# Kernel optimization log

Measured on AMD Instinct MI355X. Metric: run time of the kernel, lower is better.

The kernel has to match this reference:

```python
import jax, jax.numpy as jnp
import numpy as np

N_USERS = 100000
N_ITEMS = 50000
N_NODES = N_USERS + N_ITEMS
D = 64
N_INTENTS = 128
N_LAYERS = 2
E = 3200000
E_U = 1600000
E_I = 800000
N_MP = 2


def spmm(idx, vals, x, n):
    # sparse (n,n) COO @ dense (n,d): out[r] = sum_e vals[e] * x[c[e]] where idx=[rows;cols]
    return jax.ops.segment_sum(vals[:, None] * x[idx[1]], idx[0], num_segments=n)


def graph_conv_both(edges, h, n):
    # DGL GraphConv(norm='both', weight=None, bias=None, allow_zero_in_degree=True)
    src, dst = edges[0], edges[1]
    ones = jnp.ones(src.shape[0], h.dtype)
    deg_out = jax.ops.segment_sum(ones, src, num_segments=n)
    deg_in = jax.ops.segment_sum(ones, dst, num_segments=n)
    inv = lambda d: jnp.where(d > 0, jax.lax.rsqrt(jnp.maximum(d, 1e-12)), 0.0)
    hs = h * inv(deg_out)[:, None]
    agg = jax.ops.segment_sum(hs[src], dst, num_segments=n)
    return agg * inv(deg_in)[:, None]


def semantic_attention(z, W1, b1, w2):
    # z: (N, M, D)
    w = jnp.tanh(z @ W1 + b1) @ w2        # (N, M)
    beta = jax.nn.softmax(w.mean(0))       # (M,)
    return jnp.einsum('m,nmd->nd', beta, z)


def dccf(G_indices, G_values, feat_user, feat_item, user_intent, item_intent):
    emb = jnp.concatenate([feat_user, feat_item], axis=0)
    total = emb
    cur = emb
    for _ in range(N_LAYERS):
        gnn = spmm(G_indices, G_values, cur, N_NODES)
        u, it = cur[:N_USERS], cur[N_USERS:]
        u_int = jax.nn.softmax(u @ user_intent, axis=1) @ user_intent.T
        i_int = jax.nn.softmax(it @ item_intent, axis=1) @ item_intent.T
        cur = gnn + jnp.concatenate([u_int, i_int], axis=0) + cur
        total = total + cur
    return total[:N_USERS], total[N_USERS:]


def han(mp_edges, h, n, W1, b1, w2):
    z = jnp.stack([graph_conv_both(mp_edges[m], h, n) for m in range(N_MP)], axis=1)
    return semantic_attention(z, W1, b1, w2)


def setup_inputs() -> dict:
    key = jax.random.key(0)
    ks = jax.random.split(key, 16)
    s = 1.0 / np.sqrt(D)
    return {
        'G_indices': jax.random.randint(ks[0], (2, E), 0, N_NODES),
        'G_values': jax.random.uniform(ks[1], (E,), jnp.float32),
        'feat_user': jax.random.normal(ks[2], (N_USERS, D), jnp.float32) * s,
        'feat_item': jax.random.normal(ks[3], (N_ITEMS, D), jnp.float32) * s,
        'user_intent': jax.random.normal(ks[4], (D, N_INTENTS), jnp.float32) * s,
        'item_intent': jax.random.normal(ks[5], (D, N_INTENTS), jnp.float32) * s,
        'mp_user_edges': jax.random.randint(ks[6], (N_MP, 2, E_U), 0, N_USERS),
        'mp_item_edges': jax.random.randint(ks[7], (N_MP, 2, E_I), 0, N_ITEMS),
        'sem_user_W1': jax.random.normal(ks[8], (D, 128), jnp.float32) * s,
        'sem_user_b1': jnp.zeros((128,), jnp.float32),
        'sem_user_w2': jax.random.normal(ks[9], (128,), jnp.float32) * s,
        'sem_item_W1': jax.random.normal(ks[10], (D, 128), jnp.float32) * s,
        'sem_item_b1': jnp.zeros((128,), jnp.float32),
        'sem_item_w2': jax.random.normal(ks[11], (128,), jnp.float32) * s,
        'user_idx': jax.random.randint(ks[12], (1024,), 0, N_USERS),
        'item_idx': jax.random.randint(ks[13], (1024,), 0, N_ITEMS),
        'neg_item_idx': jax.random.randint(ks[14], (1024,), 0, N_ITEMS),
    }


def reference(G_indices, G_values, feat_user, feat_item, user_intent, item_intent,
              mp_user_edges, mp_item_edges,
              sem_user_W1, sem_user_b1, sem_user_w2,
              sem_item_W1, sem_item_b1, sem_item_w2,
              user_idx, item_idx, neg_item_idx):
    ua, ia = dccf(G_indices, G_values, feat_user, feat_item, user_intent, item_intent)
    h_user = han(mp_user_edges, feat_user, N_USERS, sem_user_W1, sem_user_b1, sem_user_w2)
    h_item = han(mp_item_edges, feat_item, N_ITEMS, sem_item_W1, sem_item_b1, sem_item_w2)
    user_emb = 0.5 * ua + 0.5 * h_user
    item_emb = 0.5 * ia + 0.5 * h_item
    return (user_emb, item_emb)
```

## Files before the change

### kernel.cpp

```cpp
#include <hip/hip_runtime.h>
#include <hip/hip_bf16.h>
#include <hip/hip_fp16.h>
#include <math.h>

#define N_USERS 100000
#define N_ITEMS 50000
#define N_NODES 150000
#define DD 64
#define E_G 3200000
#define EU 1600000
#define EI 800000
#define E_HAN 4800000
#define NH 300000
#define NBG 293
#define NBH 586
#define ROWS 32

__device__ __forceinline__ float invdeg(float d){
  return d > 0.f ? rsqrtf(fmaxf(d, 1e-12f)) : 0.f;
}
__device__ __forceinline__ float tanh_fast(float x){
  float cx = fminf(15.f, fmaxf(-15.f, x));
  float t = __expf(2.f*cx);
  return (t - 1.f)/(t + 1.f);
}
__device__ __forceinline__ unsigned short f2b(float x){
  unsigned int b = __float_as_uint(x);
  b += 0x7FFFu + ((b >> 16) & 1u);
  return (unsigned short)(b >> 16);
}
__device__ __forceinline__ float b2f(unsigned short u){
  return __uint_as_float(((unsigned int)u) << 16);
}
__device__ __forceinline__ float b2f_lo(unsigned int u){
  return __uint_as_float(u << 16);
}
__device__ __forceinline__ float b2f_hi(unsigned int u){
  return __uint_as_float(u & 0xFFFF0000u);
}
__device__ __forceinline__ unsigned short f2h(float x){
  return __half_as_ushort(__float2half(x));
}
__device__ __forceinline__ float h2f(unsigned short u){
  return __half2float(__ushort_as_half(u));
}
__device__ __forceinline__ float2 h2x2(unsigned int u){
  __half2 h = *reinterpret_cast<__half2*>(&u);
  return __half22float2(h);
}

__global__ void k_init(const float* __restrict__ fu, const float* __restrict__ fi,
                       float* __restrict__ cur, unsigned short* __restrict__ curh,
                       float* __restrict__ total){
  int i = blockIdx.x*256 + threadIdx.x;
  if (i >= N_NODES*DD) return;
  float v = (i < N_USERS*DD) ? fu[i] : fi[i - N_USERS*DD];
  cur[i] = v; total[i] = v; curh[i] = f2h(v);
}

__global__ __launch_bounds__(256) void k_colscan(int* __restrict__ wh, int nb,
                                                 int* __restrict__ colsum){
  __shared__ int s[256];
  int b = blockIdx.x, tid = threadIdx.x;
  int v = wh[tid*nb + b];
  s[tid] = v; __syncthreads();
  for (int o = 1; o < 256; o <<= 1){
    int t = (tid >= o) ? s[tid - o] : 0;
    __syncthreads();
    s[tid] += t;
    __syncthreads();
  }
  wh[tid*nb + b] = s[tid] - v;
  if (tid == 255) colsum[b] = s[255];
}

__global__ __launch_bounds__(256) void k_bscan(const int* __restrict__ colsum, int nb,
                                               int total, int* __restrict__ bB){
  __shared__ int s[256];
  __shared__ int carry;
  int tid = threadIdx.x;
  if (tid == 0) carry = 0;
  __syncthreads();
  for (int base = 0; base < nb; base += 256){
    int i = base + tid;
    int v = (i < nb) ? colsum[i] : 0;
    s[tid] = v; __syncthreads();
    for (int o = 1; o < 256; o <<= 1){
      int t = (tid >= o) ? s[tid - o] : 0;
      __syncthreads();
      s[tid] += t;
      __syncthreads();
    }
    int c = carry;
    if (i < nb) bB[i] = c + s[tid] - v;
    __syncthreads();
    if (tid == 255) carry = c + s[255];
    __syncthreads();
  }
  if (tid == 0) bB[nb] = total;
}

__global__ __launch_bounds__(256) void k_h1_g(const int* __restrict__ gi,
                                              int* __restrict__ wh){
  __shared__ int h[NBG];
  int tid = threadIdx.x;
  for (int b = tid; b < NBG; b += 256) h[b] = 0;
  __syncthreads();
  int e0 = blockIdx.x*(E_G/256);
  for (int i = tid; i < E_G/256; i += 256)
    atomicAdd(&h[gi[e0 + i] >> 9], 1);
  __syncthreads();
  for (int b = tid; b < NBG; b += 256) wh[blockIdx.x*NBG + b] = h[b];
}

__global__ __launch_bounds__(256) void k_h2_g(const int* __restrict__ gi,
        const float* __restrict__ gv, const int* __restrict__ wh,
        const int* __restrict__ bB, uint2* __restrict__ kv){
  __shared__ int lcur[NBG];
  int tid = threadIdx.x, wg = blockIdx.x;
  for (int b = tid; b < NBG; b += 256) lcur[b] = bB[b] + wh[wg*NBG + b];
  __syncthreads();
  int e0 = wg*(E_G/256);
  for (int i = tid; i < E_G/256; i += 256){
    int e = e0 + i;
    int d = gi[e];
    int p = atomicAdd(&lcur[d >> 9], 1);
    uint2 r;
    r.x = ((unsigned)(d & 511) << 18) | (unsigned)gi[E_G + e];
    r.y = __float_as_uint(gv[e]);
    kv[p] = r;
  }
}

__global__ __launch_bounds__(256) void k_p2_g(const int* __restrict__ bB,
        const uint2* __restrict__ kv, int* __restrict__ off,
        unsigned int* __restrict__ packed){
  __shared__ int cnt[512], sc[512], lcur[512];
  int b = blockIdx.x, tid = threadIdx.x;
  int d0 = b << 9;
  int dcnt = min(512, N_NODES - d0);
  int pb = bB[b], pe = bB[b+1];
  for (int i = tid; i < 512; i += 256) cnt[i] = 0;
  __syncthreads();
  for (int p = pb + tid; p < pe; p += 256)
    atomicAdd(&cnt[kv[p].x >> 18], 1);
  __syncthreads();
  sc[tid] = cnt[tid]; sc[tid + 256] = cnt[tid + 256];
  __syncthreads();
  for (int o = 1; o < 512; o <<= 1){
    int a0 = (tid >= o) ? sc[tid - o] : 0;
    int a1 = sc[tid + 256 - o];
    __syncthreads();
    sc[tid] += a0; sc[tid + 256] += a1;
    __syncthreads();
  }
  for (int i = tid; i < 512; i += 256) lcur[i] = pb + sc[i] - cnt[i];
  for (int i = tid; i < dcnt; i += 256) off[d0 + i] = pb + sc[i] - cnt[i];
  if (tid == 0) off[d0 + dcnt] = pe;
  __syncthreads();
  for (int p = pb + tid; p < pe; p += 256){
    uint2 r = kv[p];
    int dl = (int)(r.x >> 18);
    unsigned int s = r.x & 0x3FFFFu;
    float v = __uint_as_float(r.y);
    int q14 = (int)(v*16383.f + 0.5f);
    if (q14 > 16383) q14 = 16383;
    int q = atomicAdd(&lcur[dl], 1);
    packed[q] = (s << 14) | (unsigned int)q14;
  }
}

__global__ __launch_bounds__(256) void k_spmm_gp(const int* __restrict__ off,
        const unsigned int* __restrict__ packed,
        const unsigned short* __restrict__ curh, unsigned short* __restrict__ gnnh){
  int wv = threadIdx.x >> 6, lane = threadIdx.x & 63;
  int node = blockIdx.x*4 + wv;
  if (node >= N_NODES) return;
  int b = off[node], e = off[node+1];
  int c8 = (lane & 7)*8, sl = lane >> 3;
  const float inv14 = 1.f/16383.f;
  float a[8];
  #pragma unroll
  for (int j = 0; j < 8; ++j) a[j] = 0.f;
  for (int k = b; k < e; k += 16){
    int i0 = k + sl, i1 = i0 + 8;
    unsigned int pk0 = (i0 < e) ? packed[i0] : 0u;
    unsigned int pk1 = (i1 < e) ? packed[i1] : 0u;
    int s0 = (int)(pk0 >> 14), s1 = (int)(pk1 >> 14);
    float w0 = (float)(pk0 & 16383u) * inv14;
    float w1 = (float)(pk1 & 16383u) * inv14;
    const uint4 u0 = *(const uint4*)&curh[s0*DD + c8];
    const uint4 u1 = *(const uint4*)&curh[s1*DD + c8];
    float2 f;
    f = h2x2(u0.x); a[0]=fmaf(w0,f.x,a[0]); a[1]=fmaf(w0,f.y,a[1]);
    f = h2x2(u0.y); a[2]=fmaf(w0,f.x,a[2]); a[3]=fmaf(w0,f.y,a[3]);
    f = h2x2(u0.z); a[4]=fmaf(w0,f.x,a[4]); a[5]=fmaf(w0,f.y,a[5]);
    f = h2x2(u0.w); a[6]=fmaf(w0,f.x,a[6]); a[7]=fmaf(w0,f.y,a[7]);
    f = h2x2(u1.x); a[0]=fmaf(w1,f.x,a[0]); a[1]=fmaf(w1,f.y,a[1]);
    f = h2x2(u1.y); a[2]=fmaf(w1,f.x,a[2]); a[3]=fmaf(w1,f.y,a[3]);
    f = h2x2(u1.z); a[4]=fmaf(w1,f.x,a[4]); a[5]=fmaf(w1,f.y,a[5]);
    f = h2x2(u1.w); a[6]=fmaf(w1,f.x,a[6]); a[7]=fmaf(w1,f.y,a[7]);
  }
  #pragma unroll
  for (int j = 0; j < 8; ++j){
    a[j] += __shfl_xor(a[j], 8, 64);
    a[j] += __shfl_xor(a[j], 16, 64);
    a[j] += __shfl_xor(a[j], 32, 64);
  }
  if (lane < 8){
    uint4 o;
    o.x = (unsigned)f2h(a[0]) | ((unsigned)f2h(a[1]) << 16);
    o.y = (unsigned)f2h(a[2]) | ((unsigned)f2h(a[3]) << 16);
    o.z = (unsigned)f2h(a[4]) | ((unsigned)f2h(a[5]) << 16);
    o.w = (unsigned)f2h(a[6]) | ((unsigned)f2h(a[7]) << 16);
    *(uint4*)&gnnh[node*DD + c8] = o;
  }
}

__global__ __launch_bounds__(256) void k_intent2(const float* __restrict__ intent,
        const unsigned short* __restrict__ gnnh, float* __restrict__ cur,
        unsigned short* __restrict__ curh, float* __restrict__ total,
        int base, int nrows){
  __shared__ float sB[64*132];
  __shared__ float sU[ROWS*132];
  int tid = threadIdx.x, tx = tid & 15, ty = tid >> 4;

  for (int i = tid; i < 2048; i += 256){
    int r = i >> 5, c = (i & 31) << 2;
    *(float4*)&sB[r*132 + c] = *(const float4*)&intent[r*128 + c];
  }
  {
    int r = tid & 31, q0 = tid >> 5;
    int rr = blockIdx.x*ROWS + r;
    int rowg = base + (rr < nrows ? rr : nrows - 1);
    for (int q = q0; q < 16; q += 8){
      float4 v = *(const float4*)&cur[rowg*DD + 4*q];
      sU[(4*q+0)*36 + r] = v.x;
      sU[(4*q+1)*36 + r] = v.y;
      sU[(4*q+2)*36 + r] = v.z;
      sU[(4*q+3)*36 + r] = v.w;
    }
  }
  __syncthreads();

  float w[2][8];
  #pragma unroll
  for (int i = 0; i < 2; ++i)
    #pragma unroll
    for (int k = 0; k < 8; ++k) w[i][k] = 0.f;
  for (int d = 0; d < 64; ++d){
    float2 a = *(const float2*)&sU[d*36 + 2*ty];
    float4 b0 = *(const float4*)&sB[d*132 + 8*tx];
    float4 b1 = *(const float4*)&sB[d*132 + 8*tx + 4];
    float bb[8] = {b0.x,b0.y,b0.z,b0.w,b1.x,b1.y,b1.z,b1.w};
    #pragma unroll
    for (int k = 0; k < 8; ++k){ w[0][k] += a.x*bb[k]; w[1][k] += a.y*bb[k]; }
  }

  float p[2][8];
  #pragma unroll
  for (int i = 0; i < 2; ++i){
    float mx = w[i][0];
    #pragma unroll
    for (int k = 1; k < 8; ++k) mx = fmaxf(mx, w[i][k]);
    mx = fmaxf(mx, __shfl_xor(mx, 1, 64));
    mx = fmaxf(mx, __shfl_xor(mx, 2, 64));
    mx = fmaxf(mx, __shfl_xor(mx, 4, 64));
    mx = fmaxf(mx, __shfl_xor(mx, 8, 64));
    float s = 0.f;
    #pragma unroll
    for (int k = 0; k < 8; ++k){ p[i][k] = __expf(w[i][k] - mx); s += p[i][k]; }
    s += __shfl_xor(s, 1, 64);
    s += __shfl_xor(s, 2, 64);
    s += __shfl_xor(s, 4, 64);
    s += __shfl_xor(s, 8, 64);
    float inv = 1.f / s;
    #pragma unroll
    for (int k = 0; k < 8; ++k) p[i][k] *= inv;
  }
  __syncthreads();
  #pragma unroll
  for (int i = 0; i < 2; ++i){
    *(float4*)&sU[(2*ty+i)*132 + 8*tx]     = make_float4(p[i][0],p[i][1],p[i][2],p[i][3]);
    *(float4*)&sU[(2*ty+i)*132 + 8*tx + 4] = make_float4(p[i][4],p[i][5],p[i][6],p[i][7]);
  }
  __syncthreads();

  float o[2][4];
  #pragma unroll
  for (int i = 0; i < 2; ++i)
    #pragma unroll
    for (int m = 0; m < 4; ++m) o[i][m] = 0.f;
  for (int q = 0; q < 32; ++q){
    float4 p0 = *(const float4*)&sU[(2*ty+0)*132 + 4*q];
    float4 p1 = *(const float4*)&sU[(2*ty+1)*132 + 4*q];
    #pragma unroll
    for (int m = 0; m < 4; ++m){
      float4 bl = *(const float4*)&sB[(4*tx+m)*132 + 4*q];
      o[0][m] += p0.x*bl.x + p0.y*bl.y + p0.z*bl.z + p0.w*bl.w;
      o[1][m] += p1.x*bl.x + p1.y*bl.y + p1.z*bl.z + p1.w*bl.w;
    }
  }

  #pragma unroll
  for (int i = 0; i < 2; ++i){
    int rr = blockIdx.x*ROWS + 2*ty + i;
    if (rr < nrows){
      int rowg = base + rr;
      ushort4 gh = *(const ushort4*)&gnnh[rowg*DD + 4*tx];
      float4 c = *(const float4*)&cur[rowg*DD + 4*tx];
      float4 t = *(const float4*)&total[rowg*DD + 4*tx];
      float4 cn = make_float4(h2f(gh.x) + o[i][0] + c.x, h2f(gh.y) + o[i][1] + c.y,
                              h2f(gh.z) + o[i][2] + c.z, h2f(gh.w) + o[i][3] + c.w);
      *(float4*)&cur[rowg*DD + 4*tx] = cn;
      ushort4 ch;
      ch.x = f2h(cn.x); ch.y = f2h(cn.y); ch.z = f2h(cn.z); ch.w = f2h(cn.w);
      *(ushort4*)&curh[rowg*DD + 4*tx] = ch;
      *(float4*)&total[rowg*DD + 4*tx] =
          make_float4(t.x + cn.x, t.y + cn.y, t.z + cn.z, t.w + cn.w);
    }
  }
}

__device__ __forceinline__ void han_decode(int t, const int* mp_u, const int* mp_i,
                                           int* gs, int* gd){
  if (t < 2*EU){
    int s = (t < EU) ? 0 : 1;
    int e = t - s*EU;
    const int* sp = mp_u + (long)s*2*EU;
    int nb = s*N_USERS;
    *gs = nb + sp[e]; *gd = nb + sp[EU + e];
  } else {
    int t2 = t - 2*EU;
    int s = (t2 < EI) ? 0 : 1;
    int e = t2 - s*EI;
    const int* sp = mp_i + (long)s*2*EI;
    int nb = 2*N_USERS + s*N_ITEMS;
    *gs = nb + sp[e]; *gd = nb + sp[EI + e];
  }
}

__global__ __launch_bounds__(256) void k_h1_h(const int* __restrict__ mp_u,
        const int* __restrict__ mp_i, int* __restrict__ whD, int* __restrict__ whS){
  __shared__ int hd[NBH], hs[NBH];
  int tid = threadIdx.x;
  for (int b = tid; b < NBH; b += 256){ hd[b] = 0; hs[b] = 0; }
  __syncthreads();
  int t0 = blockIdx.x*(E_HAN/256);
  for (int i = tid; i < E_HAN/256; i += 256){
    int gs, gd;
    han_decode(t0 + i, mp_u, mp_i, &gs, &gd);
    atomicAdd(&hd[gd >> 9], 1);
    atomicAdd(&hs[gs >> 9], 1);
  }
  __syncthreads();
  for (int b = tid; b < NBH; b += 256){
    whD[blockIdx.x*NBH + b] = hd[b];
    whS[blockIdx.x*NBH + b] = hs[b];
  }
}

__global__ __launch_bounds__(256) void k_h2_h(const int* __restrict__ mp_u,
        const int* __restrict__ mp_i, const int* __restrict__ whD,
        const int* __restrict__ whS, const int* __restrict__ bBD,
        const int* __restrict__ bBS, unsigned int* __restrict__ keyD,
        int* __restrict__ keyS){
  __shared__ int lcD[NBH], lcS[NBH];
  int tid = threadIdx.x, wg = blockIdx.x;
  for (int b = tid; b < NBH; b += 256){
    lcD[b] = bBD[b] + whD[wg*NBH + b];
    lcS[b] = bBS[b] + whS[wg*NBH + b];
  }
  __syncthreads();
  int t0 = wg*(E_HAN/256);
  for (int i = tid; i < E_HAN/256; i += 256){
    int gs, gd;
    han_decode(t0 + i, mp_u, mp_i, &gs, &gd);
    int pD = atomicAdd(&lcD[gd >> 9], 1);
    keyD[pD] = ((unsigned)(gd & 511) << 19) | (unsigned)gs;
    int pS = atomicAdd(&lcS[gs >> 9], 1);
    keyS[pS] = gs;
  }
}

__global__ __launch_bounds__(256) void k_p2_h(const int* __restrict__ bB,
        const unsigned int* __restrict__ key, const int* __restrict__ dego,
        int* __restrict__ off, unsigned int* __restrict__ ssrc){
  __shared__ int cnt[512], sc[512], lcur[512];
  int b = blockIdx.x, tid = threadIdx.x;
  int d0 = b << 9;
  int dcnt = min(512, NH - d0);
  int pb = bB[b], pe = bB[b+1];
  for (int i = tid; i < 512; i += 256) cnt[i] = 0;
  __syncthreads();
  for (int p = pb + tid; p < pe; p += 256)
    atomicAdd(&cnt[key[p] >> 19], 1);
  __syncthreads();
  sc[tid] = cnt[tid]; sc[tid + 256] = cnt[tid + 256];
  __syncthreads();
  for (int o = 1; o < 512; o <<= 1){
    int a0 = (tid >= o) ? sc[tid - o] : 0;
    int a1 = sc[tid + 256 - o];
    __syncthreads();
    sc[tid] += a0; sc[tid + 256] += a1;
    __syncthreads();
  }
  for (int i = tid; i < 512; i += 256) lcur[i] = pb + sc[i] - cnt[i];
  for (int i = tid; i < dcnt; i += 256) off[d0 + i] = pb + sc[i] - cnt[i];
  if (tid == 0) off[d0 + dcnt] = pe;
  __syncthreads();
  for (int p = pb + tid; p < pe; p += 256){
    unsigned int k = key[p];
    int dl = (int)(k >> 19);
    int gs = (int)(k & 0x7FFFFu);
    int fsrc = gs - (gs >= N_USERS ? N_USERS : 0) - (gs >= 250000 ? 50000 : 0);
    float w = invdeg((float)dego[gs]);
    int q14 = (int)(w*16383.f + 0.5f);
    if (q14 > 16383) q14 = 16383;
    int q = atomicAdd(&lcur[dl], 1);
    ssrc[q] = ((unsigned)fsrc << 14) | (unsigned)q14;
  }
}

__global__ __launch_bounds__(256) void k_cnt_hs(const int* __restrict__ bB,
        const int* __restrict__ keyS, int* __restrict__ dego){
  __shared__ int cnt[512];
  int b = blockIdx.x, tid = threadIdx.x;
  int d0 = b << 9;
  int dcnt = min(512, NH - d0);
  int pb = bB[b], pe = bB[b+1];
  for (int i = tid; i < 512; i += 256) cnt[i] = 0;
  __syncthreads();
  for (int p = pb + tid; p < pe; p += 256)
    atomicAdd(&cnt[keyS[p] & 511], 1);
  __syncthreads();
  for (int i = tid; i < dcnt; i += 256) dego[d0 + i] = cnt[i];
}

__global__ void k_fb(const float* __restrict__ fu, const float* __restrict__ fi,
                     unsigned short* __restrict__ fb){
  int i = blockIdx.x*256 + threadIdx.x;
  if (i >= N_NODES*DD) return;
  float f = (i < N_USERS*DD) ? fu[i] : fi[i - N_USERS*DD];
  fb[i] = f2b(f);
}

__global__ __launch_bounds__(256) void k_han_gb(const int* __restrict__ off,
        const unsigned int* __restrict__ ssrc, const unsigned short* __restrict__ fb,
        unsigned short* __restrict__ zb){
  int wv = threadIdx.x >> 6, lane = threadIdx.x & 63;
  int g = blockIdx.x*4 + wv;
  if (g >= NH) return;
  int b = off[g], e = off[g+1];
  int c8 = (lane & 7)*8, sl = lane >> 3;
  const float inv14 = 1.f/16383.f;
  float a[8];
  #pragma unroll
  for (int j = 0; j < 8; ++j) a[j] = 0.f;
  for (int k = b; k < e; k += 16){
    int i0 = k + sl, i1 = i0 + 8;
    unsigned int pk0 = (i0 < e) ? ssrc[i0] : 0u;
    unsigned int pk1 = (i1 < e) ? ssrc[i1] : 0u;
    int s0 = (int)(pk0 >> 14), s1 = (int)(pk1 >> 14);
    float w0 = (float)(pk0 & 16383u) * inv14;
    float w1 = (float)(pk1 & 16383u) * inv14;
    const uint4 u0 = *(const uint4*)&fb[s0*DD + c8];
    const uint4 u1 = *(const uint4*)&fb[s1*DD + c8];
    a[0] = fmaf(w0, b2f_lo(u0.x), a[0]); a[1] = fmaf(w0, b2f_hi(u0.x), a[1]);
    a[2] = fmaf(w0, b2f_lo(u0.y), a[2]); a[3] = fmaf(w0, b2f_hi(u0.y), a[3]);
    a[4] = fmaf(w0, b2f_lo(u0.z), a[4]); a[5] = fmaf(w0, b2f_hi(u0.z), a[5]);
    a[6] = fmaf(w0, b2f_lo(u0.w), a[6]); a[7] = fmaf(w0, b2f_hi(u0.w), a[7]);
    a[0] = fmaf(w1, b2f_lo(u1.x), a[0]); a[1] = fmaf(w1, b2f_hi(u1.x), a[1]);
    a[2] = fmaf(w1, b2f_lo(u1.y), a[2]); a[3] = fmaf(w1, b2f_hi(u1.y), a[3]);
    a[4] = fmaf(w1, b2f_lo(u1.z), a[4]); a[5] = fmaf(w1, b2f_hi(u1.z), a[5]);
    a[6] = fmaf(w1, b2f_lo(u1.w), a[6]); a[7] = fmaf(w1, b2f_hi(u1.w), a[7]);
  }
  #pragma unroll
  for (int j = 0; j < 8; ++j){
    a[j] += __shfl_xor(a[j], 8, 64);
    a[j] += __shfl_xor(a[j], 16, 64);
    a[j] += __shfl_xor(a[j], 32, 64);
  }
  if (lane < 8){
    float win = invdeg((float)(e - b));
    uint4 o;
    o.x = (unsigned)f2b(win*a[0]) | ((unsigned)f2b(win*a[1]) << 16);
    o.y = (unsigned)f2b(win*a[2]) | ((unsigned)f2b(win*a[3]) << 16);
    o.z = (unsigned)f2b(win*a[4]) | ((unsigned)f2b(win*a[5]) << 16);
    o.w = (unsigned)f2b(win*a[6]) | ((unsigned)f2b(win*a[7]) << 16);
    *(uint4*)&zb[g*DD + c8] = o;
  }
}

__global__ __launch_bounds__(256) void k_sem2(const float* __restrict__ W1,
        const float* __restrict__ b1, const float* __restrict__ w2,
        const unsigned short* __restrict__ z, int nn, float* __restrict__ wsum){
  __shared__ float sW[64*132];
  __shared__ float sA[64*36];
  __shared__ float sBias[128], sV[128];
  __shared__ float red[2];
  int tid = threadIdx.x, tx = tid & 15, ty = tid >> 4;

  for (int i = tid; i < 2048; i += 256){
    int r = i >> 5, c = (i & 31) << 2;
    *(float4*)&sW[r*132 + c] = *(const float4*)&W1[r*128 + c];
  }
  if (tid < 128){ sBias[tid] = b1[tid]; sV[tid] = w2[tid]; }
  if (tid < 2) red[tid] = 0.f;

  for (int m = 0; m < 2; ++m){
    __syncthreads();
    {
      int r = tid & 31, q0 = tid >> 5;
      int rr = blockIdx.x*ROWS + r;
      int rowg = (rr < nn ? rr : nn - 1) + m*nn;
      for (int q = q0; q < 16; q += 8){
        ushort4 v = *(const ushort4*)&z[(long)rowg*DD + 4*q];
        sA[(4*q+0)*36 + r] = b2f(v.x);
        sA[(4*q+1)*36 + r] = b2f(v.y);
        sA[(4*q+2)*36 + r] = b2f(v.z);
        sA[(4*q+3)*36 + r] = b2f(v.w);
      }
    }
    __syncthreads();

    float w[2][8];
    #pragma unroll
    for (int i = 0; i < 2; ++i)
      #pragma unroll
      for (int k = 0; k < 8; ++k) w[i][k] = sBias[8*tx + k];
    for (int d = 0; d < 64; ++d){
      float2 a = *(const float2*)&sA[d*36 + 2*ty];
      float4 b0 = *(const float4*)&sW[d*132 + 8*tx];
      float4 b4 = *(const float4*)&sW[d*132 + 8*tx + 4];
      float bb[8] = {b0.x,b0.y,b0.z,b0.w,b4.x,b4.y,b4.z,b4.w};
      #pragma unroll
      for (int k = 0; k < 8; ++k){ w[0][k] += a.x*bb[k]; w[1][k] += a.y*bb[k]; }
    }
    float part = 0.f;
    #pragma unroll
    for (int i = 0; i < 2; ++i){
      int rr = blockIdx.x*ROWS + 2*ty + i;
      if (rr < nn){
        #pragma unroll
        for (int k = 0; k < 8; ++k) part += tanh_fast(w[i][k]) * sV[8*tx + k];
      }
    }
    part += __shfl_xor(part, 1, 64);
    part += __shfl_xor(part, 2, 64);
    part += __shfl_xor(part, 4, 64);
    part += __shfl_xor(part, 8, 64);
    part += __shfl_xor(part, 16, 64);
    part += __shfl_xor(part, 32, 64);
    if ((tid & 63) == 0) atomicAdd(&red[m], part);
  }
  __syncthreads();
  if (tid < 2) atomicAdd(&wsum[tid], red[tid]);
}

__global__ void k_beta(const float* __restrict__ wsum, float* __restrict__ beta){
  if (threadIdx.x == 0 && blockIdx.x == 0){
    float u0 = wsum[0] / (float)N_USERS, u1 = wsum[1] / (float)N_USERS;
    float m = fmaxf(u0, u1);
    float e0 = __expf(u0 - m), e1 = __expf(u1 - m);
    beta[0] = e0/(e0+e1); beta[1] = e1/(e0+e1);
    float i0 = wsum[2] / (float)N_ITEMS, i1 = wsum[3] / (float)N_ITEMS;
    m = fmaxf(i0, i1);
    e0 = __expf(i0 - m); e1 = __expf(i1 - m);
    beta[2] = e0/(e0+e1); beta[3] = e1/(e0+e1);
  }
}

__global__ void k_final(const float* __restrict__ total, const unsigned short* __restrict__ zb,
                        const float* __restrict__ beta, float* __restrict__ out){
  int i = blockIdx.x*256 + threadIdx.x;
  if (i >= N_NODES*DD) return;
  float h;
  if (i < N_USERS*DD)
    h = beta[0]*b2f(zb[i]) + beta[1]*b2f(zb[N_USERS*DD + i]);
  else {
    int j = i - N_USERS*DD;
    h = beta[2]*b2f(zb[2*N_USERS*DD + j]) + beta[3]*b2f(zb[(2*N_USERS + N_ITEMS)*DD + j]);
  }
  out[i] = 0.5f*total[i] + 0.5f*h;
}

extern "C" void kernel_launch(void* const* d_in, const int* in_sizes, int n_in,
                              void* d_out, int out_size, void* d_ws, size_t ws_size,
                              hipStream_t stream) {
  const int*   G_idx = (const int*)d_in[0];
  const float* G_val = (const float*)d_in[1];
  const float* fu    = (const float*)d_in[2];
  const float* fi    = (const float*)d_in[3];
  const float* u_int = (const float*)d_in[4];
  const float* i_int = (const float*)d_in[5];
  const int*   mp_u  = (const int*)d_in[6];
  const int*   mp_i  = (const int*)d_in[7];
  const float* uW1   = (const float*)d_in[8];
  const float* ub1   = (const float*)d_in[9];
  const float* uw2   = (const float*)d_in[10];
  const float* iW1   = (const float*)d_in[11];
  const float* ib1   = (const float*)d_in[12];
  const float* iw2   = (const float*)d_in[13];
  float* out = (float*)d_out;

  float* ws = (float*)d_ws;
  float*        total  = ws;
  float*        cur    = ws + 9600000;
  unsigned short* gnnh = (unsigned short*)(ws + 19200000);
  unsigned short* curh = (unsigned short*)(ws + 24000000);
  uint2*        kvG    = (uint2*)ws;
  unsigned int* packG  = (unsigned int*)(ws + 28800000);
  int*          offG   = (int*)(ws + 33700000);
  int*          whG    = (int*)(ws + 34930000);
  int*          colG   = (int*)(ws + 35018000);
  int*          bBG    = (int*)(ws + 35019000);
  unsigned int* keyH   = (unsigned int*)(ws + 9600000);
  unsigned short* zb   = (unsigned short*)(ws + 9600000);
  int*          keyS   = (int*)(ws + 19200000);
  unsigned short* fb   = (unsigned short*)(ws + 19200000);
  unsigned int* ssrcH  = (unsigned int*)(ws + 28800000);
  int*          degoH  = (int*)(ws + 34000000);
  int*          offH   = (int*)(ws + 34300000);
  int*          whH    = (int*)(ws + 34610000);
  int*          whS    = (int*)(ws + 34770000);
  int*          colH   = (int*)(ws + 35010000);
  int*          bBH    = (int*)(ws + 35012000);
  int*          colS   = (int*)(ws + 35014000);
  int*          bBS    = (int*)(ws + 35016000);
  float*        wsum   = ws + 35030000;
  float*        beta   = ws + 35030004;

  hipMemsetAsync(wsum, 0, 4*sizeof(float), stream);

  k_h1_g<<<256, 256, 0, stream>>>(G_idx, whG);
  k_colscan<<<NBG, 256, 0, stream>>>(whG, NBG, colG);
  k_bscan<<<1, 256, 0, stream>>>(colG, NBG, E_G, bBG);
  k_h2_g<<<256, 256, 0, stream>>>(G_idx, G_val, whG, bBG, kvG);
  k_p2_g<<<NBG, 256, 0, stream>>>(bBG, kvG, offG, packG);

  k_init<<<(N_NODES*DD + 255)/256, 256, 0, stream>>>(fu, fi, cur, curh, total);

  for (int layer = 0; layer < 2; ++layer){
    k_spmm_gp<<<(N_NODES + 3)/4, 256, 0, stream>>>(offG, packG, curh, gnnh);
    k_intent2<<<(N_USERS + ROWS-1)/ROWS, 256, 0, stream>>>(u_int, gnnh, cur, curh, total, 0, N_USERS);
    k_intent2<<<(N_ITEMS + ROWS-1)/ROWS, 256, 0, stream>>>(i_int, gnnh, cur, curh, total, N_USERS, N_ITEMS);
  }

  k_h1_h<<<256, 256, 0, stream>>>(mp_u, mp_i, whH, whS);
  k_colscan<<<NBH, 256, 0, stream>>>(whH, NBH, colH);
  k_bscan<<<1, 256, 0, stream>>>(colH, NBH, E_HAN, bBH);
  k_colscan<<<NBH, 256, 0, stream>>>(whS, NBH, colS);
  k_bscan<<<1, 256, 0, stream>>>(colS, NBH, E_HAN, bBS);
  k_h2_h<<<256, 256, 0, stream>>>(mp_u, mp_i, whH, whS, bBH, bBS, keyH, keyS);
  k_cnt_hs<<<NBH, 256, 0, stream>>>(bBS, keyS, degoH);
  k_fb<<<(N_NODES*DD + 255)/256, 256, 0, stream>>>(fu, fi, fb);
  k_p2_h<<<NBH, 256, 0, stream>>>(bBH, keyH, degoH, offH, ssrcH);
  k_han_gb<<<(NH + 3)/4, 256, 0, stream>>>(offH, ssrcH, fb, zb);

  k_sem2<<<(N_USERS + ROWS-1)/ROWS, 256, 0, stream>>>(uW1, ub1, uw2, zb, N_USERS, wsum);
  k_sem2<<<(N_ITEMS + ROWS-1)/ROWS, 256, 0, stream>>>(iW1, ib1, iw2,
      zb + (long)2*N_USERS*DD, N_ITEMS, wsum + 2);
  k_beta<<<1, 64, 0, stream>>>(wsum, beta);
  k_final<<<(N_NODES*DD + 255)/256, 256, 0, stream>>>(total, zb, beta, out);
}
```

Measured before the change: 1.179 ms.

## Compute HAN out-degrees with global atomics and merge user/item kernel launches

Out-degree for the HAN graphs is now counted directly with global atomics in the first histogram pass. This removes the source-side bucket sort, its two scans, the keyS scatter and the separate counting kernel. The user and item launches of the intent and semantic-attention kernels are each merged into one grid that picks its half by block index, and the SpMM accumulators are rewritten as two-wide float vectors so the compiler can emit packed FMAs. In exchange, 4.8M global atomics land on a 300K-entry degree array and an extra memset is added.

```diff
diff --git a/kernel.cpp b/kernel.cpp
--- a/kernel.cpp
+++ b/kernel.cpp
@@ -15,6 +15,10 @@
 #define NBG 293
 #define NBH 586
 #define ROWS 32
+#define NBU 3125
+#define NBI 1563
+
+typedef float v2f __attribute__((ext_vector_type(2)));
 
 __device__ __forceinline__ float invdeg(float d){
   return d > 0.f ? rsqrtf(fmaxf(d, 1e-12f)) : 0.f;
@@ -32,11 +36,11 @@
 __device__ __forceinline__ float b2f(unsigned short u){
   return __uint_as_float(((unsigned int)u) << 16);
 }
-__device__ __forceinline__ float b2f_lo(unsigned int u){
-  return __uint_as_float(u << 16);
-}
-__device__ __forceinline__ float b2f_hi(unsigned int u){
-  return __uint_as_float(u & 0xFFFF0000u);
+__device__ __forceinline__ v2f b2f2(unsigned int u){
+  v2f r;
+  r.x = __uint_as_float(u << 16);
+  r.y = __uint_as_float(u & 0xFFFF0000u);
+  return r;
 }
 __device__ __forceinline__ unsigned short f2h(float x){
   return __half_as_ushort(__float2half(x));
@@ -44,9 +48,11 @@
 __device__ __forceinline__ float h2f(unsigned short u){
   return __half2float(__ushort_as_half(u));
 }
-__device__ __forceinline__ float2 h2x2(unsigned int u){
+__device__ __forceinline__ v2f h2v2(unsigned int u){
   __half2 h = *reinterpret_cast<__half2*>(&u);
-  return __half22float2(h);
+  float2 t = __half22float2(h);
+  v2f r; r.x = t.x; r.y = t.y;
+  return r;
 }
 
 __global__ void k_init(const float* __restrict__ fu, const float* __restrict__ fi,
@@ -179,9 +185,7 @@
   int b = off[node], e = off[node+1];
   int c8 = (lane & 7)*8, sl = lane >> 3;
   const float inv14 = 1.f/16383.f;
-  float a[8];
-  #pragma unroll
-  for (int j = 0; j < 8; ++j) a[j] = 0.f;
+  v2f a0 = {0.f,0.f}, a1 = {0.f,0.f}, a2 = {0.f,0.f}, a3 = {0.f,0.f};
   for (int k = b; k < e; k += 16){
     int i0 = k + sl, i1 = i0 + 8;
     unsigned int pk0 = (i0 < e) ? packed[i0] : 0u;
@@ -191,16 +195,12 @@
     float w1 = (float)(pk1 & 16383u) * inv14;
     const uint4 u0 = *(const uint4*)&curh[s0*DD + c8];
     const uint4 u1 = *(const uint4*)&curh[s1*DD + c8];
-    float2 f;
-    f = h2x2(u0.x); a[0]=fmaf(w0,f.x,a[0]); a[1]=fmaf(w0,f.y,a[1]);
-    f = h2x2(u0.y); a[2]=fmaf(w0,f.x,a[2]); a[3]=fmaf(w0,f.y,a[3]);
-    f = h2x2(u0.z); a[4]=fmaf(w0,f.x,a[4]); a[5]=fmaf(w0,f.y,a[5]);
-    f = h2x2(u0.w); a[6]=fmaf(w0,f.x,a[6]); a[7]=fmaf(w0,f.y,a[7]);
-    f = h2x2(u1.x); a[0]=fmaf(w1,f.x,a[0]); a[1]=fmaf(w1,f.y,a[1]);
-    f = h2x2(u1.y); a[2]=fmaf(w1,f.x,a[2]); a[3]=fmaf(w1,f.y,a[3]);
-    f = h2x2(u1.z); a[4]=fmaf(w1,f.x,a[4]); a[5]=fmaf(w1,f.y,a[5]);
-    f = h2x2(u1.w); a[6]=fmaf(w1,f.x,a[6]); a[7]=fmaf(w1,f.y,a[7]);
-  }
+    a0 += w0 * h2v2(u0.x); a1 += w0 * h2v2(u0.y);
+    a2 += w0 * h2v2(u0.z); a3 += w0 * h2v2(u0.w);
+    a0 += w1 * h2v2(u1.x); a1 += w1 * h2v2(u1.y);
+    a2 += w1 * h2v2(u1.z); a3 += w1 * h2v2(u1.w);
+  }
+  float a[8] = {a0.x,a0.y,a1.x,a1.y,a2.x,a2.y,a3.x,a3.y};
   #pragma unroll
   for (int j = 0; j < 8; ++j){
     a[j] += __shfl_xor(a[j], 8, 64);
@@ -217,13 +217,17 @@
   }
 }
 
-__global__ __launch_bounds__(256) void k_intent2(const float* __restrict__ intent,
+__global__ __launch_bounds__(256) void k_intent2(const float* __restrict__ u_int,
+        const float* __restrict__ i_int,
         const unsigned short* __restrict__ gnnh, float* __restrict__ cur,
-        unsigned short* __restrict__ curh, float* __restrict__ total,
-        int base, int nrows){
+        unsigned short* __restrict__ curh, float* __restrict__ total){
   __shared__ float sB[64*132];
   __shared__ float sU[ROWS*132];
   int tid = threadIdx.x, tx = tid & 15, ty = tid >> 4;
+  int bid = blockIdx.x;
+  const float* intent; int base, nrows, lb;
+  if (bid < NBU){ intent = u_int; base = 0; nrows = N_USERS; lb = bid; }
+  else          { intent = i_int; base = N_USERS; nrows = N_ITEMS; lb = bid - NBU; }
 
   for (int i = tid; i < 2048; i += 256){
     int r = i >> 5, c = (i & 31) << 2;
@@ -231,7 +235,7 @@
   }
   {
     int r = tid & 31, q0 = tid >> 5;
-    int rr = blockIdx.x*ROWS + r;
+    int rr = lb*ROWS + r;
     int rowg = base + (rr < nrows ? rr : nrows - 1);
     for (int q = q0; q < 16; q += 8){
       float4 v = *(const float4*)&cur[rowg*DD + 4*q];
@@ -304,7 +308,7 @@
 
   #pragma unroll
   for (int i = 0; i < 2; ++i){
-    int rr = blockIdx.x*ROWS + 2*ty + i;
+    int rr = lb*ROWS + 2*ty + i;
     if (rr < nrows){
       int rowg = base + rr;
       ushort4 gh = *(const ushort4*)&gnnh[rowg*DD + 4*tx];
@@ -341,36 +345,30 @@
 }
 
 __global__ __launch_bounds__(256) void k_h1_h(const int* __restrict__ mp_u,
-        const int* __restrict__ mp_i, int* __restrict__ whD, int* __restrict__ whS){
-  __shared__ int hd[NBH], hs[NBH];
+        const int* __restrict__ mp_i, int* __restrict__ whD, int* __restrict__ dego){
+  __shared__ int hd[NBH];
   int tid = threadIdx.x;
-  for (int b = tid; b < NBH; b += 256){ hd[b] = 0; hs[b] = 0; }
+  for (int b = tid; b < NBH; b += 256) hd[b] = 0;
   __syncthreads();
   int t0 = blockIdx.x*(E_HAN/256);
   for (int i = tid; i < E_HAN/256; i += 256){
     int gs, gd;
     han_decode(t0 + i, mp_u, mp_i, &gs, &gd);
     atomicAdd(&hd[gd >> 9], 1);
-    atomicAdd(&hs[gs >> 9], 1);
-  }
-  __syncthreads();
-  for (int b = tid; b < NBH; b += 256){
+    atomicAdd(&dego[gs], 1);
+  }
+  __syncthreads();
+  for (int b = tid; b < NBH; b += 256)
     whD[blockIdx.x*NBH + b] = hd[b];
-    whS[blockIdx.x*NBH + b] = hs[b];
-  }
 }
 
 __global__ __launch_bounds__(256) void k_h2_h(const int* __restrict__ mp_u,
         const int* __restrict__ mp_i, const int* __restrict__ whD,
-        const int* __restrict__ whS, const int* __restrict__ bBD,
-        const int* __restrict__ bBS, unsigned int* __restrict__ keyD,
-        int* __restrict__ keyS){
-  __shared__ int lcD[NBH], lcS[NBH];
+        const int* __restrict__ bBD, unsigned int* __restrict__ keyD){
+  __shared__ int lcD[NBH];
   int tid = threadIdx.x, wg = blockIdx.x;
-  for (int b = tid; b < NBH; b += 256){
+  for (int b = tid; b < NBH; b += 256)
     lcD[b] = bBD[b] + whD[wg*NBH + b];
-    lcS[b] = bBS[b] + whS[wg*NBH + b];
-  }
   __syncthreads();
   int t0 = wg*(E_HAN/256);
   for (int i = tid; i < E_HAN/256; i += 256){
@@ -378,8 +376,6 @@
     han_decode(t0 + i, mp_u, mp_i, &gs, &gd);
     int pD = atomicAdd(&lcD[gd >> 9], 1);
     keyD[pD] = ((unsigned)(gd & 511) << 19) | (unsigned)gs;
-    int pS = atomicAdd(&lcS[gs >> 9], 1);
-    keyS[pS] = gs;
   }
 }
 
@@ -422,21 +418,6 @@
   }
 }
 
-__global__ __launch_bounds__(256) void k_cnt_hs(const int* __restrict__ bB,
-        const int* __restrict__ keyS, int* __restrict__ dego){
-  __shared__ int cnt[512];
-  int b = blockIdx.x, tid = threadIdx.x;
-  int d0 = b << 9;
-  int dcnt = min(512, NH - d0);
-  int pb = bB[b], pe = bB[b+1];
-  for (int i = tid; i < 512; i += 256) cnt[i] = 0;
-  __syncthreads();
-  for (int p = pb + tid; p < pe; p += 256)
-    atomicAdd(&cnt[keyS[p] & 511], 1);
-  __syncthreads();
-  for (int i = tid; i < dcnt; i += 256) dego[d0 + i] = cnt[i];
-}
-
 __global__ void k_fb(const float* __restrict__ fu, const float* __restrict__ fi,
                      unsigned short* __restrict__ fb){
   int i = blockIdx.x*256 + threadIdx.x;
@@ -454,9 +435,7 @@
   int b = off[g], e = off[g+1];
   int c8 = (lane & 7)*8, sl = lane >> 3;
   const float inv14 = 1.f/16383.f;
-  float a[8];
-  #pragma unroll
-  for (int j = 0; j < 8; ++j) a[j] = 0.f;
+  v2f a0 = {0.f,0.f}, a1 = {0.f,0.f}, a2 = {0.f,0.f}, a3 = {0.f,0.f};
   for (int k = b; k < e; k += 16){
     int i0 = k + sl, i1 = i0 + 8;
     unsigned int pk0 = (i0 < e) ? ssrc[i0] : 0u;
@@ -466,15 +445,12 @@
     float w1 = (float)(pk1 & 16383u) * inv14;
     const uint4 u0 = *(const uint4*)&fb[s0*DD + c8];
     const uint4 u1 = *(const uint4*)&fb[s1*DD + c8];
-    a[0] = fmaf(w0, b2f_lo(u0.x), a[0]); a[1] = fmaf(w0, b2f_hi(u0.x), a[1]);
-    a[2] = fmaf(w0, b2f_lo(u0.y), a[2]); a[3] = fmaf(w0, b2f_hi(u0.y), a[3]);
-    a[4] = fmaf(w0, b2f_lo(u0.z), a[4]); a[5] = fmaf(w0, b2f_hi(u0.z), a[5]);
-    a[6] = fmaf(w0, b2f_lo(u0.w), a[6]); a[7] = fmaf(w0, b2f_hi(u0.w), a[7]);
-    a[0] = fmaf(w1, b2f_lo(u1.x), a[0]); a[1] = fmaf(w1, b2f_hi(u1.x), a[1]);
-    a[2] = fmaf(w1, b2f_lo(u1.y), a[2]); a[3] = fmaf(w1, b2f_hi(u1.y), a[3]);
-    a[4] = fmaf(w1, b2f_lo(u1.z), a[4]); a[5] = fmaf(w1, b2f_hi(u1.z), a[5]);
-    a[6] = fmaf(w1, b2f_lo(u1.w), a[6]); a[7] = fmaf(w1, b2f_hi(u1.w), a[7]);
-  }
+    a0 += w0 * b2f2(u0.x); a1 += w0 * b2f2(u0.y);
+    a2 += w0 * b2f2(u0.z); a3 += w0 * b2f2(u0.w);
+    a0 += w1 * b2f2(u1.x); a1 += w1 * b2f2(u1.y);
+    a2 += w1 * b2f2(u1.z); a3 += w1 * b2f2(u1.w);
+  }
+  float a[8] = {a0.x,a0.y,a1.x,a1.y,a2.x,a2.y,a3.x,a3.y};
   #pragma unroll
   for (int j = 0; j < 8; ++j){
     a[j] += __shfl_xor(a[j], 8, 64);
@@ -492,14 +468,21 @@
   }
 }
 
-__global__ __launch_bounds__(256) void k_sem2(const float* __restrict__ W1,
-        const float* __restrict__ b1, const float* __restrict__ w2,
-        const unsigned short* __restrict__ z, int nn, float* __restrict__ wsum){
+__global__ __launch_bounds__(256) void k_sem2(const float* __restrict__ uW1,
+        const float* __restrict__ ub1, const float* __restrict__ uw2,
+        const float* __restrict__ iW1, const float* __restrict__ ib1,
+        const float* __restrict__ iw2, const unsigned short* __restrict__ zb,
+        float* __restrict__ wsum){
   __shared__ float sW[64*132];
   __shared__ float sA[64*36];
   __shared__ float sBias[128], sV[128];
   __shared__ float red[2];
   int tid = threadIdx.x, tx = tid & 15, ty = tid >> 4;
+  int bid = blockIdx.x;
+  const float *W1, *b1, *w2; const unsigned short* z; int nn, lb, wo;
+  if (bid < NBU){ W1 = uW1; b1 = ub1; w2 = uw2; z = zb; nn = N_USERS; lb = bid; wo = 0; }
+  else { W1 = iW1; b1 = ib1; w2 = iw2; z = zb + (long)2*N_USERS*DD;
+         nn = N_ITEMS; lb = bid - NBU; wo = 2; }
 
   for (int i = tid; i < 2048; i += 256){
     int r = i >> 5, c = (i & 31) << 2;
@@ -512,7 +495,7 @@
     __syncthreads();
     {
       int r = tid & 31, q0 = tid >> 5;
-      int rr = blockIdx.x*ROWS + r;
+      int rr = lb*ROWS + r;
       int rowg = (rr < nn ? rr : nn - 1) + m*nn;
       for (int q = q0; q < 16; q += 8){
         ushort4 v = *(const ushort4*)&z[(long)rowg*DD + 4*q];
@@ -540,7 +523,7 @@
     float part = 0.f;
     #pragma unroll
     for (int i = 0; i < 2; ++i){
-      int rr = blockIdx.x*ROWS + 2*ty + i;
+      int rr = lb*ROWS + 2*ty + i;
       if (rr < nn){
         #pragma unroll
         for (int k = 0; k < 8; ++k) part += tanh_fast(w[i][k]) * sV[8*tx + k];
@@ -555,7 +538,7 @@
     if ((tid & 63) == 0) atomicAdd(&red[m], part);
   }
   __syncthreads();
-  if (tid < 2) atomicAdd(&wsum[tid], red[tid]);
+  if (tid < 2) atomicAdd(&wsum[wo + tid], red[tid]);
 }
 
 __global__ void k_beta(const float* __restrict__ wsum, float* __restrict__ beta){
@@ -617,21 +600,18 @@
   int*          bBG    = (int*)(ws + 35019000);
   unsigned int* keyH   = (unsigned int*)(ws + 9600000);
   unsigned short* zb   = (unsigned short*)(ws + 9600000);
-  int*          keyS   = (int*)(ws + 19200000);
   unsigned short* fb   = (unsigned short*)(ws + 19200000);
   unsigned int* ssrcH  = (unsigned int*)(ws + 28800000);
   int*          degoH  = (int*)(ws + 34000000);
   int*          offH   = (int*)(ws + 34300000);
   int*          whH    = (int*)(ws + 34610000);
-  int*          whS    = (int*)(ws + 34770000);
   int*          colH   = (int*)(ws + 35010000);
   int*          bBH    = (int*)(ws + 35012000);
-  int*          colS   = (int*)(ws + 35014000);
-  int*          bBS    = (int*)(ws + 35016000);
   float*        wsum   = ws + 35030000;
   float*        beta   = ws + 35030004;
 
   hipMemsetAsync(wsum, 0, 4*sizeof(float), stream);
+  hipMemsetAsync(degoH, 0, NH*sizeof(int), stream);
 
   k_h1_g<<<256, 256, 0, stream>>>(G_idx, whG);
   k_colscan<<<NBG, 256, 0, stream>>>(whG, NBG, colG);
@@ -643,24 +623,18 @@
 
   for (int layer = 0; layer < 2; ++layer){
     k_spmm_gp<<<(N_NODES + 3)/4, 256, 0, stream>>>(offG, packG, curh, gnnh);
-    k_intent2<<<(N_USERS + ROWS-1)/ROWS, 256, 0, stream>>>(u_int, gnnh, cur, curh, total, 0, N_USERS);
-    k_intent2<<<(N_ITEMS + ROWS-1)/ROWS, 256, 0, stream>>>(i_int, gnnh, cur, curh, total, N_USERS, N_ITEMS);
-  }
-
-  k_h1_h<<<256, 256, 0, stream>>>(mp_u, mp_i, whH, whS);
+    k_intent2<<<NBU + NBI, 256, 0, stream>>>(u_int, i_int, gnnh, cur, curh, total);
+  }
+
+  k_h1_h<<<256, 256, 0, stream>>>(mp_u, mp_i, whH, degoH);
   k_colscan<<<NBH, 256, 0, stream>>>(whH, NBH, colH);
   k_bscan<<<1, 256, 0, stream>>>(colH, NBH, E_HAN, bBH);
-  k_colscan<<<NBH, 256, 0, stream>>>(whS, NBH, colS);
-  k_bscan<<<1, 256, 0, stream>>>(colS, NBH, E_HAN, bBS);
-  k_h2_h<<<256, 256, 0, stream>>>(mp_u, mp_i, whH, whS, bBH, bBS, keyH, keyS);
-  k_cnt_hs<<<NBH, 256, 0, stream>>>(bBS, keyS, degoH);
+  k_h2_h<<<256, 256, 0, stream>>>(mp_u, mp_i, whH, bBH, keyH);
   k_fb<<<(N_NODES*DD + 255)/256, 256, 0, stream>>>(fu, fi, fb);
   k_p2_h<<<NBH, 256, 0, stream>>>(bBH, keyH, degoH, offH, ssrcH);
   k_han_gb<<<(NH + 3)/4, 256, 0, stream>>>(offH, ssrcH, fb, zb);
 
-  k_sem2<<<(N_USERS + ROWS-1)/ROWS, 256, 0, stream>>>(uW1, ub1, uw2, zb, N_USERS, wsum);
-  k_sem2<<<(N_ITEMS + ROWS-1)/ROWS, 256, 0, stream>>>(iW1, ib1, iw2,
-      zb + (long)2*N_USERS*DD, N_ITEMS, wsum + 2);
+  k_sem2<<<NBU + NBI, 256, 0, stream>>>(uW1, ub1, uw2, iW1, ib1, iw2, zb, wsum);
   k_beta<<<1, 64, 0, stream>>>(wsum, beta);
   k_final<<<(N_NODES*DD + 255)/256, 256, 0, stream>>>(total, zb, beta, out);
 }
```

Result: slower. 1.252 ms (+6.3%).
